# Kernel tuning notes

Hardware: AMD Instinct MI355X
Metric: run time of the kernel (lower is better)

## Reference

```python
import jax, jax.numpy as jnp
import numpy as np

B, T, C, HS = 256, 256, 384, 64

def setup_inputs() -> dict:
    key = jax.random.key(0)
    ks = jax.random.split(key, 7)
    return {
        "x": jax.random.normal(ks[0], (B, T, C), dtype=jnp.float32),
        "Wq": jax.random.normal(ks[1], (C, HS), dtype=jnp.float32) * (C ** -0.5),
        "bq": jax.random.normal(ks[2], (HS,), dtype=jnp.float32) * 0.02,
        "Wk": jax.random.normal(ks[3], (C, HS), dtype=jnp.float32) * (C ** -0.5),
        "bk": jax.random.normal(ks[4], (HS,), dtype=jnp.float32) * 0.02,
        "Wv": jax.random.normal(ks[5], (C, HS), dtype=jnp.float32) * (C ** -0.5),
        "bv": jax.random.normal(ks[6], (HS,), dtype=jnp.float32) * 0.02,
    }

def reference(x, Wq, bq, Wk, bk, Wv, bv):
    # single-head causal self-attention (eval mode: dropout is identity)
    T_ = x.shape[1]
    q = x @ Wq + bq          # [B, T, HS]
    k = x @ Wk + bk          # [B, T, HS]
    v = x @ Wv + bv          # [B, T, HS]
    scale = k.shape[-1] ** -0.5
    att = jnp.einsum("btd,bsd->bts", q, k) * scale   # [B, T, T]
    causal = jnp.tril(jnp.ones((T_, T_), dtype=bool))  # tril buffer
    att = jnp.where(causal, att, -jnp.inf)             # mask future positions
    att = jax.nn.softmax(att, axis=-1)
    return jnp.einsum("bts,bsd->btd", att, v)          # [B, T, HS]
```

## Files before the change

### kernel.cpp

```cpp
#include <hip/hip_runtime.h>
#include <hip/hip_bf16.h>

#define BB 256
#define TT 256
#define CC 384
#define HSS 64

typedef __bf16 bf16_t;
typedef bf16_t bf16x8 __attribute__((ext_vector_type(8)));
typedef bf16_t bf16x4 __attribute__((ext_vector_type(4)));
typedef float f32x4 __attribute__((ext_vector_type(4)));

__device__ __forceinline__ f32x4 mfma16(bf16x8 a, bf16x8 b, f32x4 c) {
    return __builtin_amdgcn_mfma_f32_16x16x32_bf16(a, b, c, 0, 0, 0);
}

__device__ __forceinline__ bf16x8 cvt8(float4 a, float4 b) {
    bf16x8 r;
    r[0] = (bf16_t)a.x; r[1] = (bf16_t)a.y; r[2] = (bf16_t)a.z; r[3] = (bf16_t)a.w;
    r[4] = (bf16_t)b.x; r[5] = (bf16_t)b.y; r[6] = (bf16_t)b.z; r[7] = (bf16_t)b.w;
    return r;
}

typedef __attribute__((address_space(3))) unsigned int lds_uint_t;
typedef const __attribute__((address_space(1))) unsigned int glb_uint_t;
__device__ __forceinline__ void async_cp16(const void* g, void* lds_uniform) {
    __builtin_amdgcn_global_load_lds((glb_uint_t*)g, (lds_uint_t*)lds_uniform, 16, 0, 0);
}

__global__ void prep_w(const float* __restrict__ Wq, const float* __restrict__ Wk,
                       const float* __restrict__ Wv, bf16_t* __restrict__ WtG) {
    int idx = blockIdx.x * 256 + threadIdx.x;
    if (idx >= 192 * 384) return;
    int n = idx / 384, k = idx % 384;
    const float* W = (n < 64) ? Wq : (n < 128) ? Wk : Wv;
    float val = W[k * 64 + (n & 63)];
    int kc = k >> 6, kin = k & 63;
    int c = kin >> 3, e = k & 7;
    int pc = c ^ (n & 7);
    WtG[kc * 12288 + n * 64 + pc * 8 + e] = (bf16_t)val;
}

__global__ __attribute__((amdgpu_flat_work_group_size(1024, 1024),
                          amdgpu_waves_per_eu(4, 4)))
void head_fused(
    const float* __restrict__ x, const bf16_t* __restrict__ WtG,
    const float* __restrict__ bq, const float* __restrict__ bk, const float* __restrict__ bv,
    float* __restrict__ out) {

    __shared__ bf16_t Wl[2][12288];
    __shared__ uint4 Ksw[2048];
    __shared__ uint4 Vsw[2048];
    __shared__ __align__(16) bf16_t Pb[16 * 640];

    int b = blockIdx.x, tid = threadIdx.x;
    int w = tid >> 6, l = tid & 63, lr = l & 15, lq = l >> 4;
    int Mt = w;

    float bqv[4], bkv[4], bvv[4];
#pragma unroll
    for (int nt = 0; nt < 4; nt++) {
        bqv[nt] = bq[nt * 16 + lr];
        bkv[nt] = bk[nt * 16 + lr];
        bvv[nt] = bv[nt * 16 + lr];
    }

    const float* xr = x + ((size_t)b * TT + Mt * 16 + lr) * CC;

    f32x4 acc[12];
#pragma unroll
    for (int i = 0; i < 12; i++) acc[i] = (f32x4){0.f, 0.f, 0.f, 0.f};

    float4 xf[2][2];

#define DMA_CHUNK(kc, buf)                                                   \
    {                                                                        \
        const bf16_t* _src = WtG + (kc) * 12288;                             \
        int cb0 = w * 64;                                                    \
        async_cp16(_src + (size_t)(cb0 + l) * 8,                             \
                   &Wl[buf][(size_t)cb0 * 8]);                               \
        if (w < 8) {                                                         \
            int cb1 = (16 + w) * 64;                                         \
            async_cp16(_src + (size_t)(cb1 + l) * 8,                         \
                       &Wl[buf][(size_t)cb1 * 8]);                           \
        }                                                                    \
    }
#define LOAD_X(kc)                                                           \
    {                                                                        \
        _Pragma("unroll")                                                    \
        for (int t = 0; t < 2; t++) {                                        \
            const float* xp = xr + (kc) * 64 + t * 32 + lq * 8;              \
            xf[t][0] = *(const float4*)xp;                                   \
            xf[t][1] = *(const float4*)(xp + 4);                             \
        }                                                                    \
    }

    DMA_CHUNK(0, 0);
    LOAD_X(0);

#pragma unroll
    for (int kc = 0; kc < 6; kc++) {
        __syncthreads();
        bf16x8 af[2];
#pragma unroll
        for (int t = 0; t < 2; t++) af[t] = cvt8(xf[t][0], xf[t][1]);
        if (kc < 5) {
            DMA_CHUNK(kc + 1, (kc + 1) & 1);
            LOAD_X(kc + 1);
        }
        const bf16_t* buf = Wl[kc & 1];
#pragma unroll
        for (int nt = 0; nt < 12; nt++) {
            const bf16_t* wl = buf + (size_t)(nt * 16 + lr) * 64;
#pragma unroll
            for (int t = 0; t < 2; t++) {
                int pc = (t * 4 + lq) ^ (lr & 7);
                bf16x8 bfrag = *(const bf16x8*)(wl + pc * 8);
                acc[nt] = mfma16(af[t], bfrag, acc[nt]);
            }
        }
    }
#undef DMA_CHUNK
#undef LOAD_X

    bf16_t* KswB = (bf16_t*)Ksw;
    bf16_t* VswB = (bf16_t*)Vsw;
#pragma unroll
    for (int nt = 4; nt < 8; nt++) {
        int d = (nt - 4) * 16 + lr;
#pragma unroll
        for (int r = 0; r < 4; r++) {
            int s = Mt * 16 + lq * 4 + r;
            KswB[s * 64 + ((d >> 3) ^ (s & 7)) * 8 + (d & 7)] =
                (bf16_t)(acc[nt][r] + bkv[nt - 4]);
        }
    }
#pragma unroll
    for (int nt = 8; nt < 12; nt++) {
        int d = (nt - 8) * 16 + lr;
        int t0 = Mt * 16 + lq * 4;
        int c = t0 >> 3;
        bf16x4 pk;
#pragma unroll
        for (int r = 0; r < 4; r++) pk[r] = (bf16_t)(acc[nt][r] + bvv[nt - 8]);
        *(bf16x4*)(VswB + d * 256 + ((c & ~7) | ((c ^ d) & 7)) * 8 + (t0 & 7)) = pk;
    }
    __syncthreads();

    const float scale2 = 0.125f * 1.4426950408889634f;
    bf16_t* Pw = Pb + w * 640;

    int R0 = Mt * 16;
    int tg = R0 + lr;
    int ktm = Mt >> 1;

    bf16x8 qf[2];
#pragma unroll
    for (int hh = 0; hh < 2; hh++) {
#pragma unroll
        for (int u = 0; u < 2; u++) {
            int nt = 2 * hh + u;
#pragma unroll
            for (int r = 0; r < 4; r++)
                Pw[(lq * 4 + r) * 40 + u * 16 + lr] =
                    (bf16_t)(acc[nt][r] + bqv[nt]);
        }
        qf[hh] = *(const bf16x8*)(Pw + lr * 40 + lq * 8);
    }

    f32x4 oacc[4] = {};
    float sum = 0.f;
#pragma unroll
    for (int kt = 0; kt < 8; kt++) {
        if (kt <= ktm) {
#pragma unroll
            for (int u = 0; u < 2; u++) {
                int nt = kt * 2 + u;
                int s = nt * 16 + lr;
                const uint4* krow = Ksw + s * 8;
                bf16x8 k0 = __builtin_bit_cast(bf16x8, krow[lq ^ (s & 7)]);
                bf16x8 k1 = __builtin_bit_cast(bf16x8, krow[(4 + lq) ^ (s & 7)]);
                f32x4 a = {0.f, 0.f, 0.f, 0.f};
                a = mfma16(k0, qf[0], a);
                a = mfma16(k1, qf[1], a);
                bf16x4 pk;
#pragma unroll
                for (int r = 0; r < 4; r++) {
                    int sg = nt * 16 + lq * 4 + r;
                    float p = (sg <= tg) ? exp2f(a[r] * scale2) : 0.f;
                    sum += p;
                    pk[r] = (bf16_t)p;
                }
                *(bf16x4*)(Pw + lr * 40 + u * 16 + lq * 4) = pk;
            }
            bf16x8 pf = *(const bf16x8*)(Pw + lr * 40 + lq * 8);
#pragma unroll
            for (int dt = 0; dt < 4; dt++) {
                int d = dt * 16 + lr;
                int cc = kt * 4 + lq;
                bf16x8 vf = __builtin_bit_cast(bf16x8,
                    Vsw[d * 32 + ((cc & ~7) | ((cc ^ d) & 7))]);
                oacc[dt] = mfma16(vf, pf, oacc[dt]);
            }
        }
    }

    sum += __shfl_xor(sum, 16);
    sum += __shfl_xor(sum, 32);
    float inv = 1.0f / sum;

    float* orow = out + ((size_t)b * TT + R0 + lr) * HSS;
#pragma unroll
    for (int dt = 0; dt < 4; dt++) {
        float4 o;
        o.x = oacc[dt][0] * inv;
        o.y = oacc[dt][1] * inv;
        o.z = oacc[dt][2] * inv;
        o.w = oacc[dt][3] * inv;
        *(float4*)(orow + dt * 16 + lq * 4) = o;
    }
}

extern "C" void kernel_launch(void* const* d_in, const int* in_sizes, int n_in,
                              void* d_out, int out_size, void* d_ws, size_t ws_size,
                              hipStream_t stream) {
    const float* x  = (const float*)d_in[0];
    const float* Wq = (const float*)d_in[1];
    const float* bq = (const float*)d_in[2];
    const float* Wk = (const float*)d_in[3];
    const float* bk = (const float*)d_in[4];
    const float* Wv = (const float*)d_in[5];
    const float* bv = (const float*)d_in[6];
    float* out = (float*)d_out;

    bf16_t* WtG = (bf16_t*)d_ws;

    prep_w<<<288, 256, 0, stream>>>(Wq, Wk, Wv, WtG);
    head_fused<<<BB, 1024, 0, stream>>>(x, WtG, bq, bk, bv, out);
}
```

Before: 173.8 us.

## Triple-buffer weight chunks, prefetch x two ahead, balance causal rows across waves

Weight chunks now use three LDS buffers, and the first half of each x chunk is prefetched two stages ahead, which lets the loop wait for prefetches less often per iteration. The barrier is now a raw s_barrier fenced by sched_barriers. Wave-to-row mapping is changed so waves 8-15 take rows in reverse order. Bias loads are moved after the projection loop to reduce register pressure. The extra LDS buffer raises shared memory use. The raw barrier has no explicit wait on the async global-to-LDS copies, so it depends on the compiler inserting vmcnt waits correctly.

```diff
diff --git a/kernel.cpp b/kernel.cpp
--- a/kernel.cpp
+++ b/kernel.cpp
@@ -48,22 +48,14 @@
     const float* __restrict__ bq, const float* __restrict__ bk, const float* __restrict__ bv,
     float* __restrict__ out) {
 
-    __shared__ bf16_t Wl[2][12288];
+    __shared__ bf16_t Wl[3][12288];
     __shared__ uint4 Ksw[2048];
     __shared__ uint4 Vsw[2048];
     __shared__ __align__(16) bf16_t Pb[16 * 640];
 
     int b = blockIdx.x, tid = threadIdx.x;
     int w = tid >> 6, l = tid & 63, lr = l & 15, lq = l >> 4;
-    int Mt = w;
-
-    float bqv[4], bkv[4], bvv[4];
-#pragma unroll
-    for (int nt = 0; nt < 4; nt++) {
-        bqv[nt] = bq[nt * 16 + lr];
-        bkv[nt] = bk[nt * 16 + lr];
-        bvv[nt] = bv[nt * 16 + lr];
-    }
+    int Mt = (w < 8) ? w : 23 - w;
 
     const float* xr = x + ((size_t)b * TT + Mt * 16 + lr) * CC;
 
@@ -71,7 +63,8 @@
 #pragma unroll
     for (int i = 0; i < 12; i++) acc[i] = (f32x4){0.f, 0.f, 0.f, 0.f};
 
-    float4 xf[2][2];
+    float4 xh0[2][2];
+    float4 xh1[2];
 
 #define DMA_CHUNK(kc, buf)                                                   \
     {                                                                        \
@@ -85,30 +78,40 @@
                        &Wl[buf][(size_t)cb1 * 8]);                           \
         }                                                                    \
     }
-#define LOAD_X(kc)                                                           \
+#define LOAD_XH0(kc, pp)                                                     \
     {                                                                        \
-        _Pragma("unroll")                                                    \
-        for (int t = 0; t < 2; t++) {                                        \
-            const float* xp = xr + (kc) * 64 + t * 32 + lq * 8;              \
-            xf[t][0] = *(const float4*)xp;                                   \
-            xf[t][1] = *(const float4*)(xp + 4);                             \
-        }                                                                    \
+        const float* xp = xr + (kc) * 64 + lq * 8;                           \
+        xh0[pp][0] = *(const float4*)xp;                                     \
+        xh0[pp][1] = *(const float4*)(xp + 4);                               \
+    }
+#define LOAD_XH1(kc)                                                         \
+    {                                                                        \
+        const float* xp = xr + (kc) * 64 + 32 + lq * 8;                      \
+        xh1[0] = *(const float4*)xp;                                         \
+        xh1[1] = *(const float4*)(xp + 4);                                   \
     }
 
     DMA_CHUNK(0, 0);
-    LOAD_X(0);
+    LOAD_XH0(0, 0);
+    LOAD_XH1(0);
+    DMA_CHUNK(1, 1);
+    LOAD_XH0(1, 1);
 
 #pragma unroll
     for (int kc = 0; kc < 6; kc++) {
-        __syncthreads();
         bf16x8 af[2];
-#pragma unroll
-        for (int t = 0; t < 2; t++) af[t] = cvt8(xf[t][0], xf[t][1]);
-        if (kc < 5) {
-            DMA_CHUNK(kc + 1, (kc + 1) & 1);
-            LOAD_X(kc + 1);
-        }
-        const bf16_t* buf = Wl[kc & 1];
+        af[0] = cvt8(xh0[kc & 1][0], xh0[kc & 1][1]);
+        af[1] = cvt8(xh1[0], xh1[1]);
+        __builtin_amdgcn_sched_barrier(0);
+        __builtin_amdgcn_s_barrier();
+        __builtin_amdgcn_sched_barrier(0);
+        if (kc < 4) {
+            DMA_CHUNK(kc + 2, (kc + 2) % 3);
+            LOAD_XH0(kc + 2, kc & 1);
+        }
+        if (kc < 5) { LOAD_XH1(kc + 1); }
+        __builtin_amdgcn_sched_barrier(0);
+        const bf16_t* buf = Wl[kc % 3];
 #pragma unroll
         for (int nt = 0; nt < 12; nt++) {
             const bf16_t* wl = buf + (size_t)(nt * 16 + lr) * 64;
@@ -121,7 +124,16 @@
         }
     }
 #undef DMA_CHUNK
-#undef LOAD_X
+#undef LOAD_XH0
+#undef LOAD_XH1
+
+    float bqv[4], bkv[4], bvv[4];
+#pragma unroll
+    for (int nt = 0; nt < 4; nt++) {
+        bqv[nt] = bq[nt * 16 + lr];
+        bkv[nt] = bk[nt * 16 + lr];
+        bvv[nt] = bv[nt * 16 + lr];
+    }
 
     bf16_t* KswB = (bf16_t*)Ksw;
     bf16_t* VswB = (bf16_t*)Vsw;
```

New measurement: 174.8 us. About the same (+0.6%).

## Load full projection weights into LDS upfront and balance causal tiles across waves

Applied to the files above, without the earlier changes.

Replaces the per-chunk double-buffered weight DMA with a single upfront async copy of all 144KB of bf16 weights into a shared LDS pool that is later aliased for K, V and P. This removes the five per-chunk block barriers, and x loads are now double-buffered two chunks ahead in registers. The row-tile mapping for waves 8-15 is reversed (Mt = 23-w) to pair short and long causal rows, which changes the wave-to-work assignment. The cost is a large LDS footprint (147KB per block) and higher register pressure from the extra x buffers.

```diff
diff --git a/kernel.cpp b/kernel.cpp
--- a/kernel.cpp
+++ b/kernel.cpp
@@ -48,14 +48,67 @@
     const float* __restrict__ bq, const float* __restrict__ bk, const float* __restrict__ bv,
     float* __restrict__ out) {
 
-    __shared__ bf16_t Wl[2][12288];
-    __shared__ uint4 Ksw[2048];
-    __shared__ uint4 Vsw[2048];
-    __shared__ __align__(16) bf16_t Pb[16 * 640];
+    __shared__ __align__(16) unsigned char LDSpool[147456];
+    bf16_t* Wsh = (bf16_t*)LDSpool;
+    uint4* Ksw = (uint4*)LDSpool;
+    uint4* Vsw = (uint4*)(LDSpool + 32768);
+    bf16_t* Pb = (bf16_t*)(LDSpool + 65536);
 
     int b = blockIdx.x, tid = threadIdx.x;
     int w = tid >> 6, l = tid & 63, lr = l & 15, lq = l >> 4;
-    int Mt = w;
+    int Mt = (w < 8) ? w : 23 - w;
+
+    const float* xr = x + ((size_t)b * TT + Mt * 16 + lr) * CC;
+
+#pragma unroll
+    for (int j = 0; j < 9; j++) {
+        int g = w * 9 + j;
+        async_cp16(WtG + (size_t)g * 512 + (size_t)l * 8,
+                   Wsh + (size_t)g * 512);
+    }
+
+    f32x4 acc[12];
+#pragma unroll
+    for (int i = 0; i < 12; i++) acc[i] = (f32x4){0.f, 0.f, 0.f, 0.f};
+
+    float4 xa[4], xb[4];
+
+#define LOAD_XB(dst, i)                                                      \
+    {                                                                        \
+        _Pragma("unroll")                                                    \
+        for (int t = 0; t < 2; t++)                                          \
+            _Pragma("unroll")                                                \
+            for (int h = 0; h < 2; h++)                                      \
+                dst[t * 2 + h] =                                             \
+                    *(const float4*)(xr + (i) * 64 + t * 32 + lq * 8 + h * 4); \
+    }
+
+    LOAD_XB(xa, 0);
+    LOAD_XB(xb, 1);
+
+    __syncthreads();
+
+#pragma unroll
+    for (int kc = 0; kc < 6; kc++) {
+        bf16x8 af0, af1;
+        if ((kc & 1) == 0) {
+            af0 = cvt8(xa[0], xa[1]); af1 = cvt8(xa[2], xa[3]);
+            if (kc < 4) LOAD_XB(xa, kc + 2);
+        } else {
+            af0 = cvt8(xb[0], xb[1]); af1 = cvt8(xb[2], xb[3]);
+            if (kc < 4) LOAD_XB(xb, kc + 2);
+        }
+        const bf16_t* wbase = Wsh + kc * 12288;
+#pragma unroll
+        for (int nt = 0; nt < 12; nt++) {
+            const bf16_t* wl = wbase + (size_t)(nt * 16 + lr) * 64;
+            int pc0 = lq ^ (lr & 7);
+            int pc1 = (4 + lq) ^ (lr & 7);
+            acc[nt] = mfma16(af0, *(const bf16x8*)(wl + pc0 * 8), acc[nt]);
+            acc[nt] = mfma16(af1, *(const bf16x8*)(wl + pc1 * 8), acc[nt]);
+        }
+    }
+#undef LOAD_XB
 
     float bqv[4], bkv[4], bvv[4];
 #pragma unroll
@@ -65,63 +118,7 @@
         bvv[nt] = bv[nt * 16 + lr];
     }
 
-    const float* xr = x + ((size_t)b * TT + Mt * 16 + lr) * CC;
-
-    f32x4 acc[12];
-#pragma unroll
-    for (int i = 0; i < 12; i++) acc[i] = (f32x4){0.f, 0.f, 0.f, 0.f};
-
-    float4 xf[2][2];
-
-#define DMA_CHUNK(kc, buf)                                                   \
-    {                                                                        \
-        const bf16_t* _src = WtG + (kc) * 12288;                             \
-        int cb0 = w * 64;                                                    \
-        async_cp16(_src + (size_t)(cb0 + l) * 8,                             \
-                   &Wl[buf][(size_t)cb0 * 8]);                               \
-        if (w < 8) {                                                         \
-            int cb1 = (16 + w) * 64;                                         \
-            async_cp16(_src + (size_t)(cb1 + l) * 8,                         \
-                       &Wl[buf][(size_t)cb1 * 8]);                           \
-        }                                                                    \
-    }
-#define LOAD_X(kc)                                                           \
-    {                                                                        \
-        _Pragma("unroll")                                                    \
-        for (int t = 0; t < 2; t++) {                                        \
-            const float* xp = xr + (kc) * 64 + t * 32 + lq * 8;              \
-            xf[t][0] = *(const float4*)xp;                                   \
-            xf[t][1] = *(const float4*)(xp + 4);                             \
-        }                                                                    \
-    }
-
-    DMA_CHUNK(0, 0);
-    LOAD_X(0);
-
-#pragma unroll
-    for (int kc = 0; kc < 6; kc++) {
-        __syncthreads();
-        bf16x8 af[2];
-#pragma unroll
-        for (int t = 0; t < 2; t++) af[t] = cvt8(xf[t][0], xf[t][1]);
-        if (kc < 5) {
-            DMA_CHUNK(kc + 1, (kc + 1) & 1);
-            LOAD_X(kc + 1);
-        }
-        const bf16_t* buf = Wl[kc & 1];
-#pragma unroll
-        for (int nt = 0; nt < 12; nt++) {
-            const bf16_t* wl = buf + (size_t)(nt * 16 + lr) * 64;
-#pragma unroll
-            for (int t = 0; t < 2; t++) {
-                int pc = (t * 4 + lq) ^ (lr & 7);
-                bf16x8 bfrag = *(const bf16x8*)(wl + pc * 8);
-                acc[nt] = mfma16(af[t], bfrag, acc[nt]);
-            }
-        }
-    }
-#undef DMA_CHUNK
-#undef LOAD_X
+    __syncthreads();
 
     bf16_t* KswB = (bf16_t*)Ksw;
     bf16_t* VswB = (bf16_t*)Vsw;
```

Result: no change. 173.4 us (-0.2%).
